# Performance work log

Measured on AMD Instinct MI355X. Metric: run time of the kernel, lower is better.

The kernel has to match this reference:

```python
import jax, jax.numpy as jnp
import numpy as np

N = 100_000      # nodes
E = 1_600_000    # edges
F_IN = 32        # node features
F_E = 8          # edge features
H = 64           # hidden channels
L = 2            # GAT layers
NEG_SLOPE = 0.2


def setup_inputs() -> dict:
    key = jax.random.key(0)
    ks = jax.random.split(key, 20)
    s = 0.05
    return {
        "x": jax.random.normal(ks[0], (N, F_IN), jnp.float32),
        "edge_index": jax.random.randint(ks[1], (2, E), 0, N, jnp.int64),
        "edge_attr": jax.random.normal(ks[2], (E, F_E), jnp.float32),
        # node encoder
        "enc_w": jax.random.normal(ks[3], (F_IN, H), jnp.float32) * s,
        "enc_b": jnp.zeros((H,), jnp.float32),
        # GAT layers (stacked over L)
        "gat_w": jax.random.normal(ks[4], (L, H, H), jnp.float32) * s,
        "att_src": jax.random.normal(ks[5], (L, H), jnp.float32) * s,
        "att_dst": jax.random.normal(ks[6], (L, H), jnp.float32) * s,
        "edge_w": jax.random.normal(ks[7], (L, F_E, H), jnp.float32) * s,
        "att_edge": jax.random.normal(ks[8], (L, H), jnp.float32) * s,
        "gat_b": jnp.zeros((L, H), jnp.float32),
        # link predictor MLP
        "lp_w1": jax.random.normal(ks[9], (2 * H, H), jnp.float32) * s,
        "lp_b1": jnp.zeros((H,), jnp.float32),
        "lp_w2": jax.random.normal(ks[10], (H, 1), jnp.float32) * s,
        "lp_b2": jnp.zeros((1,), jnp.float32),
    }


def _gat_conv(h, src, dst, eattr, W, a_src, a_dst, We, a_edge, b):
    """PyG GATConv, heads=1, self-loops already appended to src/dst/eattr."""
    xp = h @ W                                   # [N, H]
    alpha = (
        (xp @ a_src)[src]                        # [E']
        + (xp @ a_dst)[dst]
        + (eattr @ We) @ a_edge
    )
    alpha = jnp.where(alpha > 0, alpha, NEG_SLOPE * alpha)  # leaky_relu
    # segment softmax over destination node
    m = jax.ops.segment_max(alpha, dst, num_segments=N)
    ex = jnp.exp(alpha - m[dst])
    denom = jax.ops.segment_sum(ex, dst, num_segments=N)
    w = ex / (denom[dst] + 1e-16)                # [E']
    out = jax.ops.segment_sum(w[:, None] * xp[src], dst, num_segments=N)
    return out + b


def reference(x, edge_index, edge_attr, enc_w, enc_b, gat_w, att_src, att_dst,
              edge_w, att_edge, gat_b, lp_w1, lp_b1, lp_w2, lp_b2):
    src, dst = edge_index[0], edge_index[1]
    # add self-loops (PyG GATConv default), edge_attr filled with mean
    loop = jnp.arange(N, dtype=src.dtype)
    src_sl = jnp.concatenate([src, loop])
    dst_sl = jnp.concatenate([dst, loop])
    eattr_sl = jnp.concatenate(
        [edge_attr, jnp.broadcast_to(edge_attr.mean(0), (N, F_E))], axis=0)

    h = x @ enc_w + enc_b                        # node encoder [N, H]
    for l in range(L):
        h = jax.nn.relu(_gat_conv(h, src_sl, dst_sl, eattr_sl,
                                  gat_w[l], att_src[l], att_dst[l],
                                  edge_w[l], att_edge[l], gat_b[l]))
    # decode: gather src/dst embeddings, concat, MLP, sigmoid
    ee = jnp.concatenate([h[src], h[dst]], axis=-1)   # [E, 2H]
    logits = jax.nn.relu(ee @ lp_w1 + lp_b1) @ lp_w2 + lp_b2
    return jax.nn.sigmoid(logits).squeeze(-1)         # [E]
```

## Files before the change

### kernel.cpp

```cpp
#include <hip/hip_runtime.h>
#include <hip/hip_bf16.h>
#include <math.h>

#define N_NODES 100000
#define N_EDGES 1600000
#define F_INN   32
#define F_EE    8
#define HD      64
#define E_SL    (N_EDGES + N_NODES)
#define NEG_SLOPE 0.2f
#define SCAN_BLOCK 512
#define N_SCAN_BLOCKS ((N_NODES + SCAN_BLOCK - 1) / SCAN_BLOCK)
#define NPB 32

#define NBKT 250
#define BKT_W (N_NODES / NBKT)
#define BKT_CAP 7200
#define ME_UNR 10
#define ME_BLOCKS (N_EDGES / (256 * ME_UNR))
#define PART_CH (ME_BLOCKS * 4)
#define SB_THREADS 512
#define SEL_CAP (BKT_CAP + BKT_W)

typedef int intv4 __attribute__((ext_vector_type(4)));

__device__ __forceinline__ float waveReduceSum(float v) {
#pragma unroll
    for (int off = 32; off > 0; off >>= 1) v += __shfl_down(v, off, 64);
    return v;
}
__device__ __forceinline__ float bf_lo(uint u) { return __uint_as_float(u << 16); }
__device__ __forceinline__ float bf_hi(uint u) { return __uint_as_float(u & 0xffff0000u); }
__device__ __forceinline__ uint pack_bf2(float a, float b) {
    __hip_bfloat16 ha = __float2bfloat16(a), hb = __float2bfloat16(b);
    unsigned short ua, ub;
    __builtin_memcpy(&ua, &ha, 2); __builtin_memcpy(&ub, &hb, 2);
    return (uint)ua | ((uint)ub << 16);
}

__global__ void k_init_small(const float* __restrict__ edge_w, const float* __restrict__ att_edge,
                             float* __restrict__ we_vec) {
    int t = threadIdx.x;
    if (t < 16) {
        int l = t >> 3, k = t & 7;
        const float* We = edge_w + l * F_EE * HD + k * HD;
        const float* ae = att_edge + l * HD;
        float s = 0.0f;
#pragma unroll
        for (int j = 0; j < HD; ++j) s += We[j] * ae[j];
        we_vec[l * 8 + k] = s;
    }
}

__global__ __launch_bounds__(256) void k_fuse_w(const float* __restrict__ enc_w,
                                                const float* __restrict__ enc_b,
                                                const float* __restrict__ W0,
                                                float* __restrict__ Wc, float* __restrict__ bc) {
    int t = threadIdx.x;
    for (int idx = t; idx < F_INN * HD; idx += 256) {
        int r = idx >> 6, c = idx & 63;
        float s = 0.0f;
#pragma unroll
        for (int k = 0; k < HD; ++k) s += enc_w[r * HD + k] * W0[k * HD + c];
        Wc[idx] = s;
    }
    if (t < HD) {
        float s = 0.0f;
#pragma unroll
        for (int k = 0; k < HD; ++k) s += enc_b[k] * W0[k * HD + t];
        bc[t] = s;
    }
}

__global__ __launch_bounds__(256) void k_mean_edterm(const float* __restrict__ eattr,
                                                     const int* __restrict__ src,
                                                     const int* __restrict__ dst,
                                                     const float* __restrict__ we_vec,
                                                     float* __restrict__ partials,
                                                     int* __restrict__ bkt,
                                                     int* __restrict__ bkt_cnt,
                                                     int* __restrict__ deg) {
    __shared__ float sw[16];
    __shared__ int hist[NBKT];
    __shared__ int base[NBKT];
    int t = threadIdx.x;
    if (t < 16) sw[t] = we_vec[t];
    if (t < NBKT) hist[t] = 0;
    __syncthreads();
    float p[8];
#pragma unroll
    for (int k = 0; k < 8; ++k) p[k] = 0.0f;
    int e0 = blockIdx.x * (256 * ME_UNR);
    int rs[ME_UNR]; uint rp[ME_UNR]; int rb[ME_UNR];
#pragma unroll
    for (int u = 0; u < ME_UNR; ++u) {
        int e = e0 + u * 256 + t;
        const float4* row = (const float4*)(eattr + (size_t)e * F_EE);
        float4 r0 = row[0], r1 = row[1];
        p[0] += r0.x; p[1] += r0.y; p[2] += r0.z; p[3] += r0.w;
        p[4] += r1.x; p[5] += r1.y; p[6] += r1.z; p[7] += r1.w;
        float ed0 = r0.x * sw[0] + r0.y * sw[1] + r0.z * sw[2] + r0.w * sw[3]
                  + r1.x * sw[4] + r1.y * sw[5] + r1.z * sw[6] + r1.w * sw[7];
        float ed1 = r0.x * sw[8] + r0.y * sw[9] + r0.z * sw[10] + r0.w * sw[11]
                  + r1.x * sw[12] + r1.y * sw[13] + r1.z * sw[14] + r1.w * sw[15];
        rs[u] = src[e];
        rp[u] = pack_bf2(ed0, ed1);
        int d = dst[e];
        int b = d / BKT_W;
        rb[u] = (b << 16) | (d - b * BKT_W);
        atomicAdd(&deg[d], 1);
        atomicAdd(&hist[b], 1);
    }
    __syncthreads();
    if (t < NBKT) base[t] = atomicAdd(&bkt_cnt[t], hist[t]);
    __syncthreads();
    if (t < NBKT) hist[t] = 0;
    __syncthreads();
#pragma unroll
    for (int u = 0; u < ME_UNR; ++u) {
        int e = e0 + u * 256 + t;
        int b = rb[u] >> 16, dl = rb[u] & 0xFFFF;
        int pos = base[b] + atomicAdd(&hist[b], 1);
        intv4 rec; rec[0] = rs[u]; rec[1] = (int)rp[u]; rec[2] = e; rec[3] = dl;
        __builtin_nontemporal_store(rec, (intv4*)(bkt + ((size_t)b * BKT_CAP + pos) * 4));
    }
#pragma unroll
    for (int k = 0; k < 8; ++k) p[k] = waveReduceSum(p[k]);
    int wave = t >> 6;
    if ((t & 63) == 0) {
        float* dstp = partials + ((size_t)blockIdx.x * 4 + wave) * 8;
#pragma unroll
        for (int k = 0; k < 8; ++k) dstp[k] = p[k];
    }
}

__global__ __launch_bounds__(256) void k_mean_final(const float* __restrict__ partials,
                                                    const float* __restrict__ we_vec,
                                                    uint* __restrict__ ltp) {
    __shared__ float red[256];
    __shared__ float mean8[8];
    __shared__ float lt[2];
    int t = threadIdx.x;
    int k = t & 7;
    int chunk = t >> 3;
    float s = 0.0f;
    for (int i = chunk; i < PART_CH; i += 32) s += partials[(size_t)i * 8 + k];
    red[t] = s;
    __syncthreads();
    if (t < 8) {
        float acc = 0.0f;
#pragma unroll
        for (int c = 0; c < 32; ++c) acc += red[c * 8 + t];
        mean8[t] = acc * (1.0f / N_EDGES);
    }
    __syncthreads();
    if (t < 2) {
        float acc = 0.0f;
#pragma unroll
        for (int kk = 0; kk < 8; ++kk) acc += mean8[kk] * we_vec[t * 8 + kk];
        lt[t] = acc;
    }
    __syncthreads();
    if (t == 0) ltp[0] = pack_bf2(lt[0], lt[1]);
}

__global__ void k_deg_init(int* __restrict__ deg, int* __restrict__ bkt_cnt) {
    int i = blockIdx.x * 256 + threadIdx.x;
    if (i < N_NODES) deg[i] = 1;
    if (i < NBKT) bkt_cnt[i] = 0;
}

__global__ __launch_bounds__(SCAN_BLOCK) void k_scan1(const int* __restrict__ deg,
                                                      int* __restrict__ row_ptr,
                                                      int* __restrict__ blk_sums) {
    __shared__ int sd[SCAN_BLOCK];
    int t = threadIdx.x;
    int i = blockIdx.x * SCAN_BLOCK + t;
    int v = (i < N_NODES) ? deg[i] : 0;
    sd[t] = v;
    for (int off = 1; off < SCAN_BLOCK; off <<= 1) {
        __syncthreads();
        int x = (t >= off) ? sd[t - off] : 0;
        __syncthreads();
        sd[t] += x;
    }
    __syncthreads();
    if (i < N_NODES) row_ptr[i] = sd[t] - v;
    if (t == SCAN_BLOCK - 1) blk_sums[blockIdx.x] = sd[t];
}

__global__ __launch_bounds__(256) void k_scan2(int* __restrict__ blk_sums,
                                               int* __restrict__ blk_off) {
    __shared__ int sd[256];
    int t = threadIdx.x;
    int v = (t < N_SCAN_BLOCKS) ? blk_sums[t] : 0;
    sd[t] = v;
    for (int off = 1; off < 256; off <<= 1) {
        __syncthreads();
        int x = (t >= off) ? sd[t - off] : 0;
        __syncthreads();
        sd[t] += x;
    }
    __syncthreads();
    if (t < N_SCAN_BLOCKS) blk_off[t] = sd[t] - v;
}

__global__ void k_scan3(int* __restrict__ row_ptr, const int* __restrict__ blk_off) {
    int i = blockIdx.x * 256 + threadIdx.x;
    if (i < N_NODES) row_ptr[i] += blk_off[i / SCAN_BLOCK];
    if (i == 0) row_ptr[N_NODES] = E_SL;
}

__global__ __launch_bounds__(SB_THREADS) void k_sort_build(const int* __restrict__ bkt_cnt,
                                                           const int* __restrict__ bkt,
                                                           const int* __restrict__ row_ptr,
                                                           const uint* __restrict__ ltp,
                                                           int2* __restrict__ agg,
                                                           int2* __restrict__ dec) {
    __shared__ int S[BKT_W];
    __shared__ int cur[BKT_W];
    __shared__ unsigned short sel[SEL_CAP];
    int b = blockIdx.x;
    int t = threadIdx.x;
    int cnt = bkt_cnt[b];
    const intv4* bp = (const intv4*)(bkt + (size_t)b * BKT_CAP * 4);
    if (t < BKT_W) cur[t] = 0;
    __syncthreads();
    for (int i = t; i < cnt; i += SB_THREADS) {
        intv4 v = bp[i];
        atomicAdd(&cur[v[3]], 1);
    }
    __syncthreads();
    if (t < BKT_W) S[t] = cur[t];
    for (int off = 1; off < BKT_W; off <<= 1) {
        __syncthreads();
        int x = (t >= off && t < BKT_W) ? S[t - off] : 0;
        __syncthreads();
        if (t < BKT_W) S[t] += x;
    }
    __syncthreads();
    if (t < BKT_W) {
        cur[t] = 0;
        sel[S[t] + t] = (unsigned short)(0x8000 | t);
    }
    __syncthreads();
    for (int i = t; i < cnt; i += SB_THREADS) {
        int dl = bp[i][3];
        int r = atomicAdd(&cur[dl], 1);
        int nb = (dl == 0) ? 0 : S[dl - 1];
        sel[nb + dl + r] = (unsigned short)i;
    }
    __syncthreads();
    int n0 = b * BKT_W;
    int gb = row_ptr[n0];
    int total = cnt + BKT_W;
    uint lt = ltp[0];
    for (int p = t; p < total; p += SB_THREADS) {
        unsigned short v = sel[p];
        int2 a, d2;
        if (v & 0x8000) {
            int node = n0 + (v & 0x7fff);
            a = make_int2(node, (int)lt);
            d2 = make_int2(node, -1);
        } else {
            intv4 r = bp[v];
            a = make_int2(r[0], r[1]);
            d2 = make_int2(r[0], r[2]);
        }
        agg[gb + p] = a;
        dec[gb + p] = d2;
    }
}

__global__ __launch_bounds__(256) void k_xp0(const float* __restrict__ x,
                                             const float* __restrict__ Wc,
                                             const float* __restrict__ bc,
                                             const float* __restrict__ a_src,
                                             const float* __restrict__ a_dst,
                                             __hip_bfloat16* __restrict__ xpb,
                                             float* __restrict__ s_src,
                                             float* __restrict__ s_dst) {
    __shared__ float xr[NPB * F_INN];
    int t = threadIdx.x;
    int j = t & 63, wv = t >> 6;
    float4 w[F_INN / 4];
#pragma unroll
    for (int kk = 0; kk < F_INN / 4; ++kk) {
        w[kk].x = Wc[(4 * kk + 0) * HD + j];
        w[kk].y = Wc[(4 * kk + 1) * HD + j];
        w[kk].z = Wc[(4 * kk + 2) * HD + j];
        w[kk].w = Wc[(4 * kk + 3) * HD + j];
    }
    int n0 = blockIdx.x * NPB;
    ((float4*)xr)[t] = ((const float4*)(x + (size_t)n0 * F_INN))[t];
    __syncthreads();
    float asj = a_src[j], adj = a_dst[j], bcj = bc[j];
    for (int n = wv; n < NPB; n += 4) {
        const float4* hx = (const float4*)&xr[n * F_INN];
        float acc = bcj;
#pragma unroll
        for (int kk = 0; kk < F_INN / 4; ++kk) {
            float4 hv = hx[kk];
            acc += hv.x * w[kk].x + hv.y * w[kk].y + hv.z * w[kk].z + hv.w * w[kk].w;
        }
        int node = n0 + n;
        xpb[(size_t)node * HD + j] = __float2bfloat16(acc);
        float ts = waveReduceSum(acc * asj);
        float td = waveReduceSum(acc * adj);
        if (j == 0) { s_src[node] = ts; s_dst[node] = td; }
    }
}

__global__ __launch_bounds__(256) void k_xp(const float* __restrict__ h, const float* __restrict__ W,
                                            const float* __restrict__ a_src, const float* __restrict__ a_dst,
                                            __hip_bfloat16* __restrict__ xpb, float* __restrict__ s_src,
                                            float* __restrict__ s_dst) {
    __shared__ float hr[NPB * HD];
    int t = threadIdx.x;
    int j = t & 63, wv = t >> 6;
    float4 w[HD / 4];
#pragma unroll
    for (int kk = 0; kk < HD / 4; ++kk) {
        w[kk].x = W[(4 * kk + 0) * HD + j];
        w[kk].y = W[(4 * kk + 1) * HD + j];
        w[kk].z = W[(4 * kk + 2) * HD + j];
        w[kk].w = W[(4 * kk + 3) * HD + j];
    }
    int n0 = blockIdx.x * NPB;
#pragma unroll
    for (int i = 0; i < 2; ++i)
        ((float4*)hr)[t + i * 256] = ((const float4*)(h + (size_t)n0 * HD))[t + i * 256];
    __syncthreads();
    float asj = a_src[j], adj = a_dst[j];
    for (int n = wv; n < NPB; n += 4) {
        const float4* hx = (const float4*)&hr[n * HD];
        float acc = 0.0f;
#pragma unroll
        for (int kk = 0; kk < HD / 4; ++kk) {
            float4 hv = hx[kk];
            acc += hv.x * w[kk].x + hv.y * w[kk].y + hv.z * w[kk].z + hv.w * w[kk].w;
        }
        int node = n0 + n;
        xpb[(size_t)node * HD + j] = __float2bfloat16(acc);
        float ts = waveReduceSum(acc * asj);
        float td = waveReduceSum(acc * adj);
        if (j == 0) { s_src[node] = ts; s_dst[node] = td; }
    }
}

template <int LAYER>
__global__ __launch_bounds__(256) void k_aggregate(const int* __restrict__ row_ptr,
                                                   const int2* __restrict__ agg,
                                                   const float* __restrict__ s_src,
                                                   const float* __restrict__ s_dst,
                                                   const uint2* __restrict__ xpr,
                                                   const float* __restrict__ bias,
                                                   float* __restrict__ h) {
    int t = threadIdx.x;
    int node = blockIdx.x * 4 + (t >> 6);
    int lane = t & 63;
    int g = lane >> 4, li = lane & 15;
    int start = row_ptr[node], end = row_ptr[node + 1];
    float sd = s_dst[node];
    float ax = 0.0f, ay = 0.0f, az = 0.0f, aw = 0.0f, den = 0.0f;
    int i = start;
    for (; i + 8 <= end; i += 8) {
        int2 r0 = agg[i + g];
        int2 r1 = agg[i + 4 + g];
        int sp0 = r0.x, sp1 = r1.x;
        uint2 u0 = xpr[(size_t)sp0 * 16 + li];
        uint2 u1 = xpr[(size_t)sp1 * 16 + li];
        float a0 = s_src[sp0] + sd + (LAYER == 0 ? bf_lo((uint)r0.y) : bf_hi((uint)r0.y));
        float a1 = s_src[sp1] + sd + (LAYER == 0 ? bf_lo((uint)r1.y) : bf_hi((uint)r1.y));
        a0 = a0 > 0.0f ? a0 : NEG_SLOPE * a0;
        a1 = a1 > 0.0f ? a1 : NEG_SLOPE * a1;
        float ex0 = __expf(a0), ex1 = __expf(a1);
        den += ex0 + ex1;
        ax += ex0 * bf_lo(u0.x) + ex1 * bf_lo(u1.x);
        ay += ex0 * bf_hi(u0.x) + ex1 * bf_hi(u1.x);
        az += ex0 * bf_lo(u0.y) + ex1 * bf_lo(u1.y);
        aw += ex0 * bf_hi(u0.y) + ex1 * bf_hi(u1.y);
    }
    for (; i < end; i += 4) {
        int idx = i + g;
        bool valid = idx < end;
        int2 r = agg[valid ? idx : end - 1];
        int sp = r.x;
        uint2 u = xpr[(size_t)sp * 16 + li];
        float a = s_src[sp] + sd + (LAYER == 0 ? bf_lo((uint)r.y) : bf_hi((uint)r.y));
        a = a > 0.0f ? a : NEG_SLOPE * a;
        float ex = valid ? __expf(a) : 0.0f;
        den += ex;
        ax += ex * bf_lo(u.x);
        ay += ex * bf_hi(u.x);
        az += ex * bf_lo(u.y);
        aw += ex * bf_hi(u.y);
    }
    den += __shfl_down(den, 32, 64); ax += __shfl_down(ax, 32, 64);
    ay  += __shfl_down(ay, 32, 64); az += __shfl_down(az, 32, 64);
    aw  += __shfl_down(aw, 32, 64);
    den += __shfl_down(den, 16, 64); ax += __shfl_down(ax, 16, 64);
    ay  += __shfl_down(ay, 16, 64); az += __shfl_down(az, 16, 64);
    aw  += __shfl_down(aw, 16, 64);
    if (lane < 16) {
        float inv = 1.0f / (den + 1e-16f);
        float4 b4 = ((const float4*)bias)[li];
        float4 v;
        v.x = fmaxf(ax * inv + b4.x, 0.0f);
        v.y = fmaxf(ay * inv + b4.y, 0.0f);
        v.z = fmaxf(az * inv + b4.z, 0.0f);
        v.w = fmaxf(aw * inv + b4.w, 0.0f);
        ((float4*)(h + (size_t)node * HD))[li] = v;
    }
}

__global__ __launch_bounds__(256) void k_umm(const float* __restrict__ h, const float* __restrict__ w1,
                                             __hip_bfloat16* __restrict__ u1b, float* __restrict__ u2) {
    __shared__ float hr[NPB * HD];
    int t = threadIdx.x;
    int j = t & 63, wv = t >> 6;
    float4 wa[HD / 4], wb[HD / 4];
#pragma unroll
    for (int kk = 0; kk < HD / 4; ++kk) {
        wa[kk].x = w1[(4 * kk + 0) * HD + j];
        wa[kk].y = w1[(4 * kk + 1) * HD + j];
        wa[kk].z = w1[(4 * kk + 2) * HD + j];
        wa[kk].w = w1[(4 * kk + 3) * HD + j];
        wb[kk].x = w1[(HD + 4 * kk + 0) * HD + j];
        wb[kk].y = w1[(HD + 4 * kk + 1) * HD + j];
        wb[kk].z = w1[(HD + 4 * kk + 2) * HD + j];
        wb[kk].w = w1[(HD + 4 * kk + 3) * HD + j];
    }
    int n0 = blockIdx.x * NPB;
#pragma unroll
    for (int i = 0; i < 2; ++i)
        ((float4*)hr)[t + i * 256] = ((const float4*)(h + (size_t)n0 * HD))[t + i * 256];
    __syncthreads();
    for (int n = wv; n < NPB; n += 4) {
        const float4* hx = (const float4*)&hr[n * HD];
        float a1 = 0.0f, a2 = 0.0f;
#pragma unroll
        for (int kk = 0; kk < HD / 4; ++kk) {
            float4 hv = hx[kk];
            a1 += hv.x * wa[kk].x + hv.y * wa[kk].y + hv.z * wa[kk].z + hv.w * wa[kk].w;
            a2 += hv.x * wb[kk].x + hv.y * wb[kk].y + hv.z * wb[kk].z + hv.w * wb[kk].w;
        }
        int node = n0 + n;
        u1b[(size_t)node * HD + j] = __float2bfloat16(a1);
        u2[(size_t)node * HD + j] = a2;
    }
}

__global__ __launch_bounds__(256) void k_decode_csr(const int* __restrict__ row_ptr,
                                                    const int2* __restrict__ dec,
                                                    const uint2* __restrict__ u1r,
                                                    const float* __restrict__ u2,
                                                    const float* __restrict__ b1,
                                                    const float* __restrict__ w2,
                                                    const float* __restrict__ b2,
                                                    float* __restrict__ out) {
    int t = threadIdx.x;
    int node = blockIdx.x * 4 + (t >> 6);
    int lane = t & 63;
    int g = lane >> 4, li = lane & 15;
    float4 c4 = ((const float4*)(u2 + (size_t)node * HD))[li];
    float4 b14 = ((const float4*)b1)[li];
    float4 w4 = ((const float4*)w2)[li];
    c4.x += b14.x; c4.y += b14.y; c4.z += b14.z; c4.w += b14.w;
    float bb = b2[0];
    int start = row_ptr[node], end = row_ptr[node + 1];
    int i = start;
    for (; i + 8 <= end; i += 8) {
        int2 e0 = dec[i + g];
        int2 e1 = dec[i + 4 + g];
        uint2 ua = u1r[(size_t)e0.x * 16 + li];
        uint2 ub = u1r[(size_t)e1.x * 16 + li];
        float p0 = fmaxf(bf_lo(ua.x) + c4.x, 0.0f) * w4.x
                 + fmaxf(bf_hi(ua.x) + c4.y, 0.0f) * w4.y
                 + fmaxf(bf_lo(ua.y) + c4.z, 0.0f) * w4.z
                 + fmaxf(bf_hi(ua.y) + c4.w, 0.0f) * w4.w;
        float p1 = fmaxf(bf_lo(ub.x) + c4.x, 0.0f) * w4.x
                 + fmaxf(bf_hi(ub.x) + c4.y, 0.0f) * w4.y
                 + fmaxf(bf_lo(ub.y) + c4.z, 0.0f) * w4.z
                 + fmaxf(bf_hi(ub.y) + c4.w, 0.0f) * w4.w;
#pragma unroll
        for (int off = 8; off > 0; off >>= 1) {
            p0 += __shfl_down(p0, off, 16);
            p1 += __shfl_down(p1, off, 16);
        }
        if (li == 0) {
            if (e0.y >= 0) out[e0.y] = 1.0f / (1.0f + __expf(-(p0 + bb)));
            if (e1.y >= 0) out[e1.y] = 1.0f / (1.0f + __expf(-(p1 + bb)));
        }
    }
    for (; i < end; i += 4) {
        int idx = i + g;
        bool valid = idx < end;
        int2 e = dec[valid ? idx : end - 1];
        uint2 u = u1r[(size_t)e.x * 16 + li];
        float p = fmaxf(bf_lo(u.x) + c4.x, 0.0f) * w4.x
                + fmaxf(bf_hi(u.x) + c4.y, 0.0f) * w4.y
                + fmaxf(bf_lo(u.y) + c4.z, 0.0f) * w4.z
                + fmaxf(bf_hi(u.y) + c4.w, 0.0f) * w4.w;
#pragma unroll
        for (int off = 8; off > 0; off >>= 1) p += __shfl_down(p, off, 16);
        if (li == 0 && valid && e.y >= 0)
            out[e.y] = 1.0f / (1.0f + __expf(-(p + bb)));
    }
}

extern "C" void kernel_launch(void* const* d_in, const int* in_sizes, int n_in,
                              void* d_out, int out_size, void* d_ws, size_t ws_size,
                              hipStream_t stream) {
    const float* x        = (const float*)d_in[0];
    const int*   eidx     = (const int*)d_in[1];
    const float* eattr    = (const float*)d_in[2];
    const float* enc_w    = (const float*)d_in[3];
    const float* enc_b    = (const float*)d_in[4];
    const float* gat_w    = (const float*)d_in[5];
    const float* att_src  = (const float*)d_in[6];
    const float* att_dst  = (const float*)d_in[7];
    const float* edge_w   = (const float*)d_in[8];
    const float* att_edge = (const float*)d_in[9];
    const float* gat_b    = (const float*)d_in[10];
    const float* lp_w1    = (const float*)d_in[11];
    const float* lp_b1    = (const float*)d_in[12];
    const float* lp_w2    = (const float*)d_in[13];
    const float* lp_b2    = (const float*)d_in[14];
    float* out = (float*)d_out;

    const int* src = eidx;
    const int* dst = eidx + N_EDGES;

    float* ws = (float*)d_ws;
    float*  h       = ws;
    int*    bkt     = (int*)h;
    __hip_bfloat16* xpb = (__hip_bfloat16*)(h + (size_t)N_NODES * HD);
    int2*   agg     = (int2*)((char*)xpb + (size_t)N_NODES * HD * 2);
    int2*   dec     = agg + E_SL;
    float*  fsmall    = (float*)(dec + E_SL);
    float*  s_src     = fsmall;
    float*  s_dst     = s_src + N_NODES;
    float*  partials  = s_dst + N_NODES;
    float*  we_vec    = partials + PART_CH * 8;
    uint*   ltp       = (uint*)(we_vec + 16);
    float*  Wc        = (float*)(ltp + 1);
    float*  bc        = Wc + F_INN * HD;
    int*    row_ptr   = (int*)(bc + HD);
    int*    deg       = row_ptr + N_NODES + 1;
    int*    blk_sums  = deg + N_NODES;
    int*    blk_off   = blk_sums + N_SCAN_BLOCKS;
    int*    bkt_cnt   = blk_off + N_SCAN_BLOCKS;

    const int NB_N256 = (N_NODES + 255) / 256;
    const int NB_AGG  = N_NODES / 4;
    const int NB_DENSE = N_NODES / NPB;

    k_init_small<<<1, 64, 0, stream>>>(edge_w, att_edge, we_vec);
    k_fuse_w<<<1, 256, 0, stream>>>(enc_w, enc_b, gat_w, Wc, bc);
    k_deg_init<<<NB_N256, 256, 0, stream>>>(deg, bkt_cnt);
    k_mean_edterm<<<ME_BLOCKS, 256, 0, stream>>>(eattr, src, dst, we_vec,
                                                 partials, bkt, bkt_cnt, deg);
    k_mean_final<<<1, 256, 0, stream>>>(partials, we_vec, ltp);

    k_scan1<<<N_SCAN_BLOCKS, SCAN_BLOCK, 0, stream>>>(deg, row_ptr, blk_sums);
    k_scan2<<<1, 256, 0, stream>>>(blk_sums, blk_off);
    k_scan3<<<NB_N256, 256, 0, stream>>>(row_ptr, blk_off);
    k_sort_build<<<NBKT, SB_THREADS, 0, stream>>>(bkt_cnt, bkt, row_ptr, ltp, agg, dec);

    k_xp0<<<NB_DENSE, 256, 0, stream>>>(x, Wc, bc, att_src, att_dst, xpb, s_src, s_dst);
    k_aggregate<0><<<NB_AGG, 256, 0, stream>>>(row_ptr, agg, s_src, s_dst,
                                               (const uint2*)xpb, gat_b, h);
    k_xp<<<NB_DENSE, 256, 0, stream>>>(h, gat_w + HD * HD, att_src + HD, att_dst + HD,
                                       xpb, s_src, s_dst);
    k_aggregate<1><<<NB_AGG, 256, 0, stream>>>(row_ptr, agg, s_src, s_dst,
                                               (const uint2*)xpb, gat_b + HD, h);

    k_umm<<<NB_DENSE, 256, 0, stream>>>(h, lp_w1, xpb, h);
    k_decode_csr<<<NB_AGG, 256, 0, stream>>>(row_ptr, dec, (const uint2*)xpb, h,
                                             lp_b1, lp_w2, lp_b2, out);
}
```

Before: 526.3 us.

## Build CSR row pointers from bucket counts and stage bucket records in LDS

Drops the per-node global degree atomics and the three-kernel node-level scan. Row pointers are now derived inside the bucket sort from per-bucket local counts plus a single 250-entry bucket scan. The edge bucketing kernel first groups its records by bucket in shared memory and then writes each bucket contiguously, instead of scattering nontemporal stores. This saves kernel launches and global atomic traffic, but costs about 40KB of LDS per block, which can lower occupancy, and adds a capacity clamp that silently drops overflow edges.

```diff
diff --git a/kernel.cpp b/kernel.cpp
--- a/kernel.cpp
+++ b/kernel.cpp
@@ -9,20 +9,17 @@
 #define HD      64
 #define E_SL    (N_EDGES + N_NODES)
 #define NEG_SLOPE 0.2f
-#define SCAN_BLOCK 512
-#define N_SCAN_BLOCKS ((N_NODES + SCAN_BLOCK - 1) / SCAN_BLOCK)
 #define NPB 32
 
 #define NBKT 250
 #define BKT_W (N_NODES / NBKT)
 #define BKT_CAP 7200
 #define ME_UNR 10
-#define ME_BLOCKS (N_EDGES / (256 * ME_UNR))
+#define ME_CHUNK (256 * ME_UNR)
+#define ME_BLOCKS (N_EDGES / ME_CHUNK)
 #define PART_CH (ME_BLOCKS * 4)
 #define SB_THREADS 512
 #define SEL_CAP (BKT_CAP + BKT_W)
-
-typedef int intv4 __attribute__((ext_vector_type(4)));
 
 __device__ __forceinline__ float waveReduceSum(float v) {
 #pragma unroll
@@ -72,17 +69,23 @@
     }
 }
 
+__global__ void k_zero(int* __restrict__ bkt_pos) {
+    int t = threadIdx.x;
+    if (t < NBKT) bkt_pos[t] = 0;
+}
+
 __global__ __launch_bounds__(256) void k_mean_edterm(const float* __restrict__ eattr,
                                                      const int* __restrict__ src,
                                                      const int* __restrict__ dst,
                                                      const float* __restrict__ we_vec,
                                                      float* __restrict__ partials,
                                                      int* __restrict__ bkt,
-                                                     int* __restrict__ bkt_cnt,
-                                                     int* __restrict__ deg) {
+                                                     int* __restrict__ bkt_pos) {
     __shared__ float sw[16];
     __shared__ int hist[NBKT];
-    __shared__ int base[NBKT];
+    __shared__ int lstart[256];
+    __shared__ int gstart[NBKT];
+    __shared__ int recs[ME_CHUNK * 4];
     int t = threadIdx.x;
     if (t < 16) sw[t] = we_vec[t];
     if (t < NBKT) hist[t] = 0;
@@ -90,7 +93,7 @@
     float p[8];
 #pragma unroll
     for (int k = 0; k < 8; ++k) p[k] = 0.0f;
-    int e0 = blockIdx.x * (256 * ME_UNR);
+    int e0 = blockIdx.x * ME_CHUNK;
     int rs[ME_UNR]; uint rp[ME_UNR]; int rb[ME_UNR];
 #pragma unroll
     for (int u = 0; u < ME_UNR; ++u) {
@@ -108,27 +111,46 @@
         int d = dst[e];
         int b = d / BKT_W;
         rb[u] = (b << 16) | (d - b * BKT_W);
-        atomicAdd(&deg[d], 1);
         atomicAdd(&hist[b], 1);
     }
     __syncthreads();
-    if (t < NBKT) base[t] = atomicAdd(&bkt_cnt[t], hist[t]);
-    __syncthreads();
-    if (t < NBKT) hist[t] = 0;
+    lstart[t] = (t < NBKT) ? hist[t] : 0;
+    __syncthreads();
+    for (int off = 1; off < 256; off <<= 1) {
+        int x = (t >= off) ? lstart[t - off] : 0;
+        __syncthreads();
+        lstart[t] += x;
+        __syncthreads();
+    }
+    if (t < NBKT) {
+        int v = hist[t];
+        gstart[t] = atomicAdd(&bkt_pos[t], v);
+        lstart[t] -= v;
+        hist[t] = 0;
+    }
     __syncthreads();
 #pragma unroll
     for (int u = 0; u < ME_UNR; ++u) {
+        int b = rb[u] >> 16, dl = rb[u] & 0xFFFF;
+        int l = atomicAdd(&hist[b], 1);
         int e = e0 + u * 256 + t;
-        int b = rb[u] >> 16, dl = rb[u] & 0xFFFF;
-        int pos = base[b] + atomicAdd(&hist[b], 1);
-        intv4 rec; rec[0] = rs[u]; rec[1] = (int)rp[u]; rec[2] = e; rec[3] = dl;
-        __builtin_nontemporal_store(rec, (intv4*)(bkt + ((size_t)b * BKT_CAP + pos) * 4));
+        ((int4*)recs)[lstart[b] + l] = make_int4(rs[u], (int)rp[u], e, dl);
+    }
+    __syncthreads();
+    int w = t >> 6, lane = t & 63;
+    int4* gb4 = (int4*)bkt;
+    for (int b = w; b < NBKT; b += 4) {
+        int n = hist[b];
+        int ls = lstart[b];
+        int gs = gstart[b];
+        for (int off = lane; off < n; off += 64)
+            if (gs + off < BKT_CAP)
+                gb4[(size_t)b * BKT_CAP + gs + off] = ((const int4*)recs)[ls + off];
     }
 #pragma unroll
     for (int k = 0; k < 8; ++k) p[k] = waveReduceSum(p[k]);
-    int wave = t >> 6;
     if ((t & 63) == 0) {
-        float* dstp = partials + ((size_t)blockIdx.x * 4 + wave) * 8;
+        float* dstp = partials + ((size_t)blockIdx.x * 4 + w) * 8;
 #pragma unroll
         for (int k = 0; k < 8; ++k) dstp[k] = p[k];
     }
@@ -164,71 +186,42 @@
     if (t == 0) ltp[0] = pack_bf2(lt[0], lt[1]);
 }
 
-__global__ void k_deg_init(int* __restrict__ deg, int* __restrict__ bkt_cnt) {
-    int i = blockIdx.x * 256 + threadIdx.x;
-    if (i < N_NODES) deg[i] = 1;
-    if (i < NBKT) bkt_cnt[i] = 0;
-}
-
-__global__ __launch_bounds__(SCAN_BLOCK) void k_scan1(const int* __restrict__ deg,
-                                                      int* __restrict__ row_ptr,
-                                                      int* __restrict__ blk_sums) {
-    __shared__ int sd[SCAN_BLOCK];
-    int t = threadIdx.x;
-    int i = blockIdx.x * SCAN_BLOCK + t;
-    int v = (i < N_NODES) ? deg[i] : 0;
+__global__ void k_bktscan(const int* __restrict__ bkt_pos, int* __restrict__ bktbase,
+                          int* __restrict__ row_ptr) {
+    __shared__ int sd[256];
+    int t = threadIdx.x;
+    int v = (t < NBKT) ? min(bkt_pos[t], BKT_CAP) + BKT_W : 0;
     sd[t] = v;
-    for (int off = 1; off < SCAN_BLOCK; off <<= 1) {
-        __syncthreads();
+    __syncthreads();
+    for (int off = 1; off < 256; off <<= 1) {
         int x = (t >= off) ? sd[t - off] : 0;
         __syncthreads();
         sd[t] += x;
-    }
-    __syncthreads();
-    if (i < N_NODES) row_ptr[i] = sd[t] - v;
-    if (t == SCAN_BLOCK - 1) blk_sums[blockIdx.x] = sd[t];
-}
-
-__global__ __launch_bounds__(256) void k_scan2(int* __restrict__ blk_sums,
-                                               int* __restrict__ blk_off) {
-    __shared__ int sd[256];
-    int t = threadIdx.x;
-    int v = (t < N_SCAN_BLOCKS) ? blk_sums[t] : 0;
-    sd[t] = v;
-    for (int off = 1; off < 256; off <<= 1) {
         __syncthreads();
-        int x = (t >= off) ? sd[t - off] : 0;
-        __syncthreads();
-        sd[t] += x;
-    }
-    __syncthreads();
-    if (t < N_SCAN_BLOCKS) blk_off[t] = sd[t] - v;
-}
-
-__global__ void k_scan3(int* __restrict__ row_ptr, const int* __restrict__ blk_off) {
-    int i = blockIdx.x * 256 + threadIdx.x;
-    if (i < N_NODES) row_ptr[i] += blk_off[i / SCAN_BLOCK];
-    if (i == 0) row_ptr[N_NODES] = E_SL;
-}
-
-__global__ __launch_bounds__(SB_THREADS) void k_sort_build(const int* __restrict__ bkt_cnt,
+    }
+    if (t < NBKT) bktbase[t] = sd[t] - v;
+    if (t == 0) row_ptr[N_NODES] = E_SL;
+}
+
+__global__ __launch_bounds__(SB_THREADS) void k_sort_build(const int* __restrict__ bkt_pos,
                                                            const int* __restrict__ bkt,
-                                                           const int* __restrict__ row_ptr,
+                                                           const int* __restrict__ bktbase,
                                                            const uint* __restrict__ ltp,
                                                            int2* __restrict__ agg,
-                                                           int2* __restrict__ dec) {
+                                                           int2* __restrict__ dec,
+                                                           int* __restrict__ row_ptr) {
     __shared__ int S[BKT_W];
     __shared__ int cur[BKT_W];
     __shared__ unsigned short sel[SEL_CAP];
     int b = blockIdx.x;
     int t = threadIdx.x;
-    int cnt = bkt_cnt[b];
-    const intv4* bp = (const intv4*)(bkt + (size_t)b * BKT_CAP * 4);
+    int cnt = min(bkt_pos[b], BKT_CAP);
+    const int4* bp = (const int4*)bkt + (size_t)b * BKT_CAP;
     if (t < BKT_W) cur[t] = 0;
     __syncthreads();
     for (int i = t; i < cnt; i += SB_THREADS) {
-        intv4 v = bp[i];
-        atomicAdd(&cur[v[3]], 1);
+        int4 v = bp[i];
+        atomicAdd(&cur[v.w], 1);
     }
     __syncthreads();
     if (t < BKT_W) S[t] = cur[t];
@@ -239,20 +232,21 @@
         if (t < BKT_W) S[t] += x;
     }
     __syncthreads();
+    int n0 = b * BKT_W;
+    int gb = bktbase[b];
     if (t < BKT_W) {
+        row_ptr[n0 + t] = gb + (t == 0 ? 0 : S[t - 1]) + t;
         cur[t] = 0;
         sel[S[t] + t] = (unsigned short)(0x8000 | t);
     }
     __syncthreads();
     for (int i = t; i < cnt; i += SB_THREADS) {
-        int dl = bp[i][3];
+        int dl = bp[i].w;
         int r = atomicAdd(&cur[dl], 1);
         int nb = (dl == 0) ? 0 : S[dl - 1];
         sel[nb + dl + r] = (unsigned short)i;
     }
     __syncthreads();
-    int n0 = b * BKT_W;
-    int gb = row_ptr[n0];
     int total = cnt + BKT_W;
     uint lt = ltp[0];
     for (int p = t; p < total; p += SB_THREADS) {
@@ -263,9 +257,9 @@
             a = make_int2(node, (int)lt);
             d2 = make_int2(node, -1);
         } else {
-            intv4 r = bp[v];
-            a = make_int2(r[0], r[1]);
-            d2 = make_int2(r[0], r[2]);
+            int4 r = bp[v];
+            a = make_int2(r.x, r.y);
+            d2 = make_int2(r.x, r.z);
         }
         agg[gb + p] = a;
         dec[gb + p] = d2;
@@ -547,26 +541,22 @@
     float*  Wc        = (float*)(ltp + 1);
     float*  bc        = Wc + F_INN * HD;
     int*    row_ptr   = (int*)(bc + HD);
-    int*    deg       = row_ptr + N_NODES + 1;
-    int*    blk_sums  = deg + N_NODES;
-    int*    blk_off   = blk_sums + N_SCAN_BLOCKS;
-    int*    bkt_cnt   = blk_off + N_SCAN_BLOCKS;
-
-    const int NB_N256 = (N_NODES + 255) / 256;
+    int*    bkt_pos   = row_ptr + N_NODES + 1;
+    int*    bktbase   = bkt_pos + NBKT;
+
     const int NB_AGG  = N_NODES / 4;
     const int NB_DENSE = N_NODES / NPB;
 
     k_init_small<<<1, 64, 0, stream>>>(edge_w, att_edge, we_vec);
     k_fuse_w<<<1, 256, 0, stream>>>(enc_w, enc_b, gat_w, Wc, bc);
-    k_deg_init<<<NB_N256, 256, 0, stream>>>(deg, bkt_cnt);
+    k_zero<<<1, 256, 0, stream>>>(bkt_pos);
     k_mean_edterm<<<ME_BLOCKS, 256, 0, stream>>>(eattr, src, dst, we_vec,
-                                                 partials, bkt, bkt_cnt, deg);
+                                                 partials, bkt, bkt_pos);
     k_mean_final<<<1, 256, 0, stream>>>(partials, we_vec, ltp);
 
-    k_scan1<<<N_SCAN_BLOCKS, SCAN_BLOCK, 0, stream>>>(deg, row_ptr, blk_sums);
-    k_scan2<<<1, 256, 0, stream>>>(blk_sums, blk_off);
-    k_scan3<<<NB_N256, 256, 0, stream>>>(row_ptr, blk_off);
-    k_sort_build<<<NBKT, SB_THREADS, 0, stream>>>(bkt_cnt, bkt, row_ptr, ltp, agg, dec);
+    k_bktscan<<<1, 256, 0, stream>>>(bkt_pos, bktbase, row_ptr);
+    k_sort_build<<<NBKT, SB_THREADS, 0, stream>>>(bkt_pos, bkt, bktbase, ltp,
+                                                  agg, dec, row_ptr);
 
     k_xp0<<<NB_DENSE, 256, 0, stream>>>(x, Wc, bc, att_src, att_dst, xpb, s_src, s_dst);
     k_aggregate<0><<<NB_AGG, 256, 0, stream>>>(row_ptr, agg, s_src, s_dst,
```

Measured after the change: 468.3 us. 11.0% less time.
